# Kernel tuning notes

Measured on AMD Instinct MI355X. Metric: run time of the kernel, lower is better.

## Reference

```python
import jax, jax.numpy as jnp
import numpy as np

H = 16      # query heads
KV = 8      # kv heads
D = 128     # head_dim
HID = 2048  # hidden_size
T = 2048    # tokens
EPS = 1e-6
THETA = 1000000.0


def setup_inputs() -> dict:
    key = jax.random.key(0)
    ks = jax.random.split(key, 4)
    return {
        "hidden_states": jax.random.normal(ks[0], (T, HID), jnp.float32),
        "positions": jnp.arange(T, dtype=jnp.int32),
        "qkv_w": jax.random.normal(ks[1], (H * D + 2 * KV * D, HID), jnp.float32) * 0.02,
        "o_w": jax.random.normal(ks[2], (HID, H * D), jnp.float32) * 0.02,
        "q_norm_w": jnp.ones((D,), jnp.float32),
        "k_norm_w": jnp.ones((D,), jnp.float32),
    }


def _rmsnorm(x, w):
    # x: [T, heads, D]; normalize over last dim
    var = jnp.mean(x * x, axis=-1, keepdims=True)
    return x * jax.lax.rsqrt(var + EPS) * w


def _rope(x, positions):
    # neox-style rotate-half; x: [T, heads, D]
    half = D // 2
    inv_freq = 1.0 / (THETA ** (jnp.arange(0, half, dtype=jnp.float32) / half * 1.0))
    inv_freq = 1.0 / (THETA ** (jnp.arange(0, D, 2, dtype=jnp.float32) / D))
    ang = positions.astype(jnp.float32)[:, None] * inv_freq  # [T, D/2]
    cos = jnp.cos(ang)[:, None, :]
    sin = jnp.sin(ang)[:, None, :]
    x1, x2 = x[..., :half], x[..., half:]
    return jnp.concatenate([x1 * cos - x2 * sin, x2 * cos + x1 * sin], axis=-1)


def reference(hidden_states, positions, qkv_w, o_w, q_norm_w, k_norm_w):
    scale = D ** -0.5
    qkv = hidden_states @ qkv_w.T  # [T, H*D + 2*KV*D]
    q = qkv[:, : H * D].reshape(T, H, D)
    k = qkv[:, H * D : H * D + KV * D].reshape(T, KV, D)
    v = qkv[:, H * D + KV * D :].reshape(T, KV, D)

    q = _rope(_rmsnorm(q, q_norm_w), positions)
    k = _rope(_rmsnorm(k, k_norm_w), positions)

    # GQA: repeat kv heads to match query heads
    rep = H // KV
    k = jnp.repeat(k, rep, axis=1)  # [T, H, D]
    v = jnp.repeat(v, rep, axis=1)

    scores = jnp.einsum("thd,shd->hts", q, k) * scale  # [H, T, T]
    causal = positions[:, None] >= positions[None, :]  # [T, T]
    scores = jnp.where(causal[None, :, :], scores, jnp.float32(-1e30))
    p = jax.nn.softmax(scores, axis=-1)
    o = jnp.einsum("hts,shd->thd", p, v).reshape(T, H * D)
    return o @ o_w.T  # [T, HID]
```

## Files before the change

### kernel.cpp

```cpp
#include <hip/hip_runtime.h>
#include <math.h>

#define T_TOK 2048
#define HID 2048
#define NH 16
#define NKV 8
#define HD 128
#define QKV_N 4096
#define EPS 1e-6f

typedef unsigned short u16;
typedef unsigned int   u32;
typedef __attribute__((ext_vector_type(8))) u16   u16x8;
typedef __attribute__((ext_vector_type(8))) short short8;
typedef __attribute__((ext_vector_type(4))) float floatx4;
typedef __attribute__((ext_vector_type(4))) u32   u32x4;

__device__ __forceinline__ u16 f2bf(float x) {
    u32 u = __float_as_uint(x);
    u = (u + 0x7fffu + ((u >> 16) & 1u)) >> 16;
    return (u16)u;
}
__device__ __forceinline__ float bf2f(u16 h) {
    return __uint_as_float(((u32)h) << 16);
}

__global__ __launch_bounds__(256) void cvt_f32_bf16(
    const float* __restrict__ in, u16* __restrict__ out)
{
    const size_t i = ((size_t)blockIdx.x * 256 + threadIdx.x) * 8;
    float4 a = *(const float4*)(in + i);
    float4 b = *(const float4*)(in + i + 4);
    u16x8 o;
    o[0] = f2bf(a.x); o[1] = f2bf(a.y); o[2] = f2bf(a.z); o[3] = f2bf(a.w);
    o[4] = f2bf(b.x); o[5] = f2bf(b.y); o[6] = f2bf(b.z); o[7] = f2bf(b.w);
    *(u16x8*)(out + i) = o;
}

template<bool OUT_BF16>
__global__ __launch_bounds__(256) void gemm_bt_bf16(
    const u16* __restrict__ A, const u16* __restrict__ B,
    void* __restrict__ Cv, int K, int lda, int ldb, int ldc)
{
    __shared__ short As[128 * 32];
    __shared__ short Bs[128 * 32];

    const int tid = threadIdx.x;
    const int w   = tid >> 6;
    const int l   = tid & 63;
    const int m0  = blockIdx.y * 128;
    const int n0  = blockIdx.x * 128;
    const int wm  = (w >> 1) * 64;
    const int wn  = (w & 1) * 64;
    const int lm  = l & 15;
    const int ko8 = (l >> 4) * 8;

    const u16* gA0 = A + (size_t)(m0      + (tid >> 2)) * lda + (tid & 3) * 8;
    const u16* gA1 = A + (size_t)(m0 + 64 + (tid >> 2)) * lda + (tid & 3) * 8;
    const u16* gB0 = B + (size_t)(n0      + (tid >> 2)) * ldb + (tid & 3) * 8;
    const u16* gB1 = B + (size_t)(n0 + 64 + (tid >> 2)) * ldb + (tid & 3) * 8;
    short* lA0 = As + w * 512;
    short* lA1 = As + 2048 + w * 512;
    short* lB0 = Bs + w * 512;
    short* lB1 = Bs + 2048 + w * 512;

    floatx4 acc[4][4];
    #pragma unroll
    for (int i = 0; i < 4; ++i)
        #pragma unroll
        for (int j = 0; j < 4; ++j) acc[i][j] = (floatx4){0.f, 0.f, 0.f, 0.f};

    for (int k0 = 0; k0 < K; k0 += 32) {
        __syncthreads();
        __builtin_amdgcn_global_load_lds(
            (const __attribute__((address_space(1))) u32*)(gA0 + k0),
            (__attribute__((address_space(3))) u32*)lA0, 16, 0, 0);
        __builtin_amdgcn_global_load_lds(
            (const __attribute__((address_space(1))) u32*)(gA1 + k0),
            (__attribute__((address_space(3))) u32*)lA1, 16, 0, 0);
        __builtin_amdgcn_global_load_lds(
            (const __attribute__((address_space(1))) u32*)(gB0 + k0),
            (__attribute__((address_space(3))) u32*)lB0, 16, 0, 0);
        __builtin_amdgcn_global_load_lds(
            (const __attribute__((address_space(1))) u32*)(gB1 + k0),
            (__attribute__((address_space(3))) u32*)lB1, 16, 0, 0);
        __syncthreads();

        short8 af[4], bfr[4];
        #pragma unroll
        for (int i = 0; i < 4; ++i)
            af[i] = *(const short8*)(As + (wm + i * 16 + lm) * 32 + ko8);
        #pragma unroll
        for (int j = 0; j < 4; ++j)
            bfr[j] = *(const short8*)(Bs + (wn + j * 16 + lm) * 32 + ko8);
        #pragma unroll
        for (int i = 0; i < 4; ++i)
            #pragma unroll
            for (int j = 0; j < 4; ++j)
                acc[i][j] = __builtin_amdgcn_mfma_f32_16x16x32_bf16(
                    af[i], bfr[j], acc[i][j], 0, 0, 0);
    }

    const int r0 = (l >> 4) * 4;
    #pragma unroll
    for (int i = 0; i < 4; ++i)
        #pragma unroll
        for (int j = 0; j < 4; ++j)
            #pragma unroll
            for (int r = 0; r < 4; ++r) {
                const int row = m0 + wm + i * 16 + r0 + r;
                const int col = n0 + wn + j * 16 + lm;
                if (OUT_BF16)
                    ((u16*)Cv)[(size_t)row * ldc + col] = f2bf(acc[i][j][r]);
                else
                    ((float*)Cv)[(size_t)row * ldc + col] = acc[i][j][r];
            }
}

__global__ __launch_bounds__(256) void prep(
    u16* __restrict__ qkv, const int* __restrict__ positions,
    const float* __restrict__ qw, const float* __restrict__ kw,
    u16* __restrict__ Kp, u16* __restrict__ Vtp)
{
    const int tile = blockIdx.x, kvh = blockIdx.y;
    const int tid = threadIdx.x;
    const int w = tid >> 6, l = tid & 63;
    const int t0 = tile * 64;

    const float qw0 = qw[2*l], qw1 = qw[2*l+1];
    const float kw0 = kw[2*l], kw1 = kw[2*l+1];
    const int   i0  = (2*l) & 63;
    const float if0 = exp2f(-(float)i0     * 0.311430758895690f);
    const float if1 = exp2f(-(float)(i0+1) * 0.311430758895690f);

    for (int rr = w; rr < 64; rr += 4) {
        const int t = t0 + rr;
        const int pos = positions[t];
        const float a0 = (float)pos * if0;
        const float a1 = (float)pos * if1;
        const float s0 = sinf(a0), c0 = cosf(a0);
        const float s1 = sinf(a1), c1 = cosf(a1);

        #pragma unroll
        for (int pass = 0; pass < 3; ++pass) {
            const int off = (pass < 2) ? (2*kvh + pass)*HD : NH*HD + kvh*HD;
            const float w0 = (pass < 2) ? qw0 : kw0;
            const float w1 = (pass < 2) ? qw1 : kw1;
            u16* p = qkv + (size_t)t*QKV_N + off;

            const u32 pk = *(const u32*)(p + 2*l);
            const float x0 = bf2f((u16)pk), x1 = bf2f((u16)(pk >> 16));
            float ss = x0*x0 + x1*x1;
            #pragma unroll
            for (int x = 1; x < 64; x <<= 1) ss += __shfl_xor(ss, x);
            const float rs = rsqrtf(ss * (1.0f/128.0f) + EPS);
            const float xn0 = x0 * rs * w0, xn1 = x1 * rs * w1;
            const float px0 = __shfl_xor(xn0, 32);
            const float px1 = __shfl_xor(xn1, 32);

            float o0, o1;
            if (l < 32) { o0 = xn0*c0 - px0*s0; o1 = xn1*c1 - px1*s1; }
            else        { o0 = xn0*c0 + px0*s0; o1 = xn1*c1 + px1*s1; }
            const u32 outpk = (u32)f2bf(o0) | ((u32)f2bf(o1) << 16);

            if (pass < 2) {
                *(u32*)(p + 2*l) = outpk;
            } else {
                const int ch = l >> 2;
                u16* dst = Kp + ((size_t)(kvh*32 + tile)*64 + rr)*128
                              + (ch ^ (rr & 15))*8 + (l & 3)*2;
                *(u32*)dst = outpk;
            }
        }
    }

    __shared__ u16 tl[64][136];
    {
        const int t  = tid >> 2;
        const int c0 = (tid & 3) * 32;
        const u16* src = qkv + (size_t)(t0 + t)*QKV_N + NH*HD + NKV*HD + kvh*HD + c0;
        #pragma unroll
        for (int p2 = 0; p2 < 4; ++p2)
            *(u16x8*)(&tl[t][c0 + p2*8]) = *(const u16x8*)(src + p2*8);
    }
    __syncthreads();
    {
        u16* dstb = Vtp + (size_t)(kvh*32 + tile) * 128 * 64;
        #pragma unroll
        for (int i = 0; i < 4; ++i) {
            const int id = tid*4 + i;
            const int d = id >> 3;
            const int o = id & 7;
            const int sb = (o ^ (d & 7)) * 8;
            u16x8 v;
            #pragma unroll
            for (int j = 0; j < 8; ++j) v[j] = tl[sb + j][d];
            *(u16x8*)(dstb + d*64 + o*8) = v;
        }
    }
}

__global__ __launch_bounds__(512) void attn_mfma(
    const u16* __restrict__ qkv, const u16* __restrict__ Kp,
    const u16* __restrict__ Vtp,
    u16* __restrict__ Opart, float2* __restrict__ ml)
{
    const int id   = blockIdx.x;
    const int half = id >> 8;
    const int kvh  = id & 7;
    const int bid  = (id & 255) >> 3;
    const int qt   = half ? bid : 31 - bid;
    const int t0   = qt * 64;
    const int tid  = threadIdx.x;
    const int w    = tid >> 6;
    const int l    = tid & 63;
    const int q4   = l >> 4;
    const int c    = l & 15;
    const int h    = kvh*2 + (w >> 2);
    const int wq   = w & 3;

    __shared__ short Ks[2][64 * 128];
    __shared__ short Vts[2][128 * 64];

    short8 bq[4];
    {
        const u16* qrow = qkv + (size_t)(t0 + wq*16 + c) * QKV_N + h*HD;
        #pragma unroll
        for (int kk = 0; kk < 4; ++kk)
            bq[kk] = *(const short8*)(qrow + kk*32 + q4*8);
    }

    float m_run = -3.0e38f, l_run = 0.f;
    floatx4 accO[8];
    #pragma unroll
    for (int db = 0; db < 8; ++db) accO[db] = (floatx4){0.f, 0.f, 0.f, 0.f};

    const float Cs = 0.12751744f;

    const int nt  = qt + 1;
    const int nh0 = (nt + 1) >> 1;
    const int tlo = half ? nh0 : 0;
    const int thi = half ? nt  : nh0;

    auto issue = [&](int tile, int buf) {
        const size_t tb = (size_t)(kvh*32 + tile) * 8192;
        const u16* g = (w < 4 ? Kp + tb + w*2048 : Vtp + tb + (w-4)*2048) + l*8;
        short* p = (w < 4) ? (Ks[buf] + w*2048) : (Vts[buf] + (w-4)*2048);
        #pragma unroll
        for (int i = 0; i < 4; ++i)
            __builtin_amdgcn_global_load_lds(
                (const __attribute__((address_space(1))) u32*)(g + i*512),
                (__attribute__((address_space(3))) u32*)(p + i*512), 16, 0, 0);
    };

    if (tlo < thi) issue(tlo, 0);
    int cur = 0;

    for (int tile = tlo; tile < thi; ++tile) {
        __syncthreads();
        if (tile + 1 < thi) issue(tile + 1, cur ^ 1);

        const short* Kc = Ks[cur];
        const short* Vc = Vts[cur];

        floatx4 accS[4];
        #pragma unroll
        for (int sb = 0; sb < 4; ++sb) accS[sb] = (floatx4){0.f, 0.f, 0.f, 0.f};
        #pragma unroll
        for (int kk = 0; kk < 4; ++kk) {
            #pragma unroll
            for (int sb = 0; sb < 4; ++sb) {
                short8 ak = *(const short8*)(Kc + (sb*16 + c)*128 + ((kk*4 + q4) ^ c)*8);
                accS[sb] = __builtin_amdgcn_mfma_f32_16x16x32_bf16(ak, bq[kk], accS[sb], 0, 0, 0);
            }
        }

        if (tile == qt) {
            #pragma unroll
            for (int sb = 0; sb < 4; ++sb)
                #pragma unroll
                for (int r = 0; r < 4; ++r) {
                    const int s_loc = sb*16 + q4*4 + r;
                    const int t_loc = wq*16 + c;
                    if (s_loc > t_loc) accS[sb][r] = -1.0e30f;
                }
        }

        float mt = -3.0e38f;
        #pragma unroll
        for (int sb = 0; sb < 4; ++sb)
            #pragma unroll
            for (int r = 0; r < 4; ++r) mt = fmaxf(mt, accS[sb][r]);
        mt = fmaxf(mt, __shfl_xor(mt, 16));
        mt = fmaxf(mt, __shfl_xor(mt, 32));

        const float m_new = fmaxf(m_run, mt);
        const float alpha = exp2f((m_run - m_new) * Cs);
        m_run = m_new;

        float P[4][4];
        float lsum = 0.f;
        #pragma unroll
        for (int sb = 0; sb < 4; ++sb)
            #pragma unroll
            for (int r = 0; r < 4; ++r) {
                const float e = exp2f((accS[sb][r] - m_new) * Cs);
                P[sb][r] = e;
                lsum += e;
            }
        lsum += __shfl_xor(lsum, 16);
        lsum += __shfl_xor(lsum, 32);
        l_run = l_run * alpha + lsum;

        #pragma unroll
        for (int r = 0; r < 4; ++r) {
            const float ar = __shfl(alpha, (l & 48) | (q4*4 + r));
            #pragma unroll
            for (int db = 0; db < 8; ++db) accO[db][r] *= ar;
        }

        u32 Pp[4][2];
        #pragma unroll
        for (int sb = 0; sb < 4; ++sb)
            #pragma unroll
            for (int p = 0; p < 2; ++p)
                Pp[sb][p] = (u32)f2bf(P[sb][2*p]) | ((u32)f2bf(P[sb][2*p+1]) << 16);

        const int src0 = ((2*q4    ) & 3) * 16 + c;
        const int src1 = ((2*q4 + 1) & 3) * 16 + c;
        const bool hiq = q4 >= 2;
        #pragma unroll
        for (int k2 = 0; k2 < 2; ++k2) {
            u32 x0 = __shfl(Pp[2*k2][0],   src0), y0 = __shfl(Pp[2*k2+1][0], src0);
            u32 x1 = __shfl(Pp[2*k2][1],   src0), y1 = __shfl(Pp[2*k2+1][1], src0);
            u32 x2 = __shfl(Pp[2*k2][0],   src1), y2 = __shfl(Pp[2*k2+1][0], src1);
            u32 x3 = __shfl(Pp[2*k2][1],   src1), y3 = __shfl(Pp[2*k2+1][1], src1);
            u32x4 av;
            av.x = hiq ? y0 : x0;  av.y = hiq ? y1 : x1;
            av.z = hiq ? y2 : x2;  av.w = hiq ? y3 : x3;
            const short8 aP = __builtin_bit_cast(short8, av);
            #pragma unroll
            for (int db = 0; db < 8; ++db) {
                short8 bv = *(const short8*)(Vc + (db*16 + c)*64 + (((k2*4 + q4) ^ (c & 7)))*8);
                accO[db] = __builtin_amdgcn_mfma_f32_16x16x32_bf16(aP, bv, accO[db], 0, 0, 0);
            }
        }
        cur ^= 1;
    }

    const size_t pbase = (size_t)(half * NH + h) * T_TOK;
    #pragma unroll
    for (int r = 0; r < 4; ++r) {
        const int qloc = q4*4 + r;
        const float mr = __shfl(m_run, (l & 48) | qloc);
        const float lr = __shfl(l_run, (l & 48) | qloc);
        const int row_g = t0 + wq*16 + qloc;
        u16* op = Opart + (pbase + row_g) * HD;
        #pragma unroll
        for (int db = 0; db < 8; ++db)
            op[db*16 + c] = f2bf(accO[db][r]);
        if (c == 0) ml[pbase + row_g] = make_float2(mr, lr);
    }
}

__global__ __launch_bounds__(256) void attn_combine(
    const u16* __restrict__ Opart, const float2* __restrict__ ml,
    u16* __restrict__ qkv)
{
    const int idx = blockIdx.x * 256 + threadIdx.x;
    const int c16 = idx & 15;
    const int t   = (idx >> 4) & (T_TOK - 1);
    const int h   = idx >> 15;
    const size_t iA = (size_t)h * T_TOK + t;
    const size_t iB = (size_t)(NH + h) * T_TOK + t;
    const float2 a = ml[iA];
    const float2 b = ml[iB];
    const float Cs = 0.12751744f;
    const float mM = fmaxf(a.x, b.x);
    const float wA = exp2f((a.x - mM) * Cs);
    const float wB = exp2f((b.x - mM) * Cs);
    const float inv = 1.0f / (wA * a.y + wB * b.y);
    const u16x8 A = *(const u16x8*)(Opart + iA * HD + c16*8);
    const u16x8 B = *(const u16x8*)(Opart + iB * HD + c16*8);
    u16x8 o;
    #pragma unroll
    for (int j = 0; j < 8; ++j)
        o[j] = f2bf((wA * bf2f(A[j]) + wB * bf2f(B[j])) * inv);
    *(u16x8*)(qkv + (size_t)t * QKV_N + h * HD + c16*8) = o;
}

extern "C" void kernel_launch(void* const* d_in, const int* in_sizes, int n_in,
                              void* d_out, int out_size, void* d_ws, size_t ws_size,
                              hipStream_t stream)
{
    const float* hidden    = (const float*)d_in[0];
    const int*   positions = (const int*)  d_in[1];
    const float* qkv_w     = (const float*)d_in[2];
    const float* o_w       = (const float*)d_in[3];
    const float* q_norm_w  = (const float*)d_in[4];
    const float* k_norm_w  = (const float*)d_in[5];
    float* out = (float*)d_out;

    u16* qkvbf = (u16*)d_ws;
    u16* wbf   = qkvbf + (size_t)T_TOK * QKV_N;
    u16* abf   = wbf   + (size_t)QKV_N * HID;
    u16* kpb   = abf   + (size_t)T_TOK * HID;
    u16* vpb   = kpb   + (size_t)NKV * T_TOK * HD;

    cvt_f32_bf16<<<(T_TOK*HID)/2048, 256, 0, stream>>>(hidden, abf);
    cvt_f32_bf16<<<(QKV_N*HID)/2048, 256, 0, stream>>>(qkv_w, wbf);

    gemm_bt_bf16<true><<<dim3(QKV_N/128, T_TOK/128), 256, 0, stream>>>(
        abf, wbf, qkvbf, HID, HID, HID, QKV_N);

    prep<<<dim3(T_TOK/64, NKV), 256, 0, stream>>>(
        qkvbf, positions, q_norm_w, k_norm_w, kpb, vpb);

    attn_mfma<<<512, 512, 0, stream>>>(qkvbf, kpb, vpb, wbf, (float2*)abf);

    attn_combine<<<(NH*T_TOK*16)/256, 256, 0, stream>>>(
        wbf, (const float2*)abf, qkvbf);

    cvt_f32_bf16<<<(HID*HID)/2048, 256, 0, stream>>>(o_w, abf);
    gemm_bt_bf16<false><<<dim3(HID/128, T_TOK/128), 256, 0, stream>>>(
        qkvbf, abf, out, HID, QKV_N, HID, HID);
}
```

Before: 285.9 us.

## Replace GEMM with 256x128 triple-buffered, swizzled, 8-wave pipelined kernel

```diff
diff --git a/kernel.cpp b/kernel.cpp
--- a/kernel.cpp
+++ b/kernel.cpp
@@ -37,83 +37,137 @@
     *(u16x8*)(out + i) = o;
 }
 
+#define GBM 256
+#define GBN 128
+#define GBK 64
+#define BUFSH 24576
+
+#define WAITV6 asm volatile("s_waitcnt vmcnt(6)" ::: "memory")
+#define WAITV0 asm volatile("s_waitcnt vmcnt(0)" ::: "memory")
+#define LGKM0  asm volatile("s_waitcnt lgkmcnt(0)" ::: "memory")
+#define BARR   asm volatile("s_barrier" ::: "memory")
+#define SB     __builtin_amdgcn_sched_barrier(0)
+
+#define STAGEU(i, tt, dstb) \
+    __builtin_amdgcn_global_load_lds( \
+        (const __attribute__((address_space(1))) u32*)(gsrc[i] + (size_t)(tt)*GBK), \
+        (__attribute__((address_space(3))) u32*)((dstb) + loff[i]), 16, 0, 0)
+
+#define RD_A(dst, srcb, f) do { \
+    dst[0] = *(const short8*)((srcb) + arow + (f)*1024 + achunk0); \
+    dst[1] = *(const short8*)((srcb) + arow + (f)*1024 + achunk1); } while (0)
+
+#define RD_B(dst, srcb) do { \
+    _Pragma("unroll") \
+    for (int j_ = 0; j_ < 4; ++j_) { \
+        dst[j_][0] = *(const short8*)((srcb) + 16384 + brow + j_*1024 + achunk0); \
+        dst[j_][1] = *(const short8*)((srcb) + 16384 + brow + j_*1024 + achunk1); } } while (0)
+
+#define MM(f, aa, bb) do { \
+    __builtin_amdgcn_s_setprio(1); \
+    _Pragma("unroll") \
+    for (int j_ = 0; j_ < 4; ++j_) { \
+        acc[f][j_] = __builtin_amdgcn_mfma_f32_16x16x32_bf16(aa[0], bb[j_][0], acc[f][j_], 0, 0, 0); \
+        acc[f][j_] = __builtin_amdgcn_mfma_f32_16x16x32_bf16(aa[1], bb[j_][1], acc[f][j_], 0, 0, 0); } \
+    __builtin_amdgcn_s_setprio(0); } while (0)
+
+#define TILE(t, CURB, NXTB, THDB, BBC, BBN) do { \
+    const bool st_ = (t) + 2 < nt; \
+    if (st_) { STAGEU(0, (t)+2, THDB); STAGEU(1, (t)+2, THDB); } \
+    RD_A(aP1, CURB, 1); SB; \
+    MM(0, aP0, BBC); SB; \
+    if (st_) { STAGEU(2, (t)+2, THDB); STAGEU(3, (t)+2, THDB); } \
+    RD_A(aP0, CURB, 2); SB; \
+    MM(1, aP1, BBC); SB; \
+    if (st_) { STAGEU(4, (t)+2, THDB); STAGEU(5, (t)+2, THDB); } \
+    RD_A(aP1, CURB, 3); SB; \
+    MM(2, aP0, BBC); \
+    if ((t) + 1 < nt) { \
+        if (st_) { WAITV6; } else { WAITV0; } \
+        LGKM0; BARR; SB; \
+        RD_B(BBN, NXTB); RD_A(aP0, NXTB, 0); \
+    } \
+    SB; \
+    MM(3, aP1, BBC); SB; \
+} while (0)
+
 template<bool OUT_BF16>
-__global__ __launch_bounds__(256) void gemm_bt_bf16(
+__global__ __launch_bounds__(512, 2) void gemm_bt_8p(
     const u16* __restrict__ A, const u16* __restrict__ B,
     void* __restrict__ Cv, int K, int lda, int ldb, int ldc)
 {
-    __shared__ short As[128 * 32];
-    __shared__ short Bs[128 * 32];
-
+    extern __shared__ short lds[];
     const int tid = threadIdx.x;
-    const int w   = tid >> 6;
-    const int l   = tid & 63;
-    const int m0  = blockIdx.y * 128;
-    const int n0  = blockIdx.x * 128;
-    const int wm  = (w >> 1) * 64;
-    const int wn  = (w & 1) * 64;
-    const int lm  = l & 15;
-    const int ko8 = (l >> 4) * 8;
-
-    const u16* gA0 = A + (size_t)(m0      + (tid >> 2)) * lda + (tid & 3) * 8;
-    const u16* gA1 = A + (size_t)(m0 + 64 + (tid >> 2)) * lda + (tid & 3) * 8;
-    const u16* gB0 = B + (size_t)(n0      + (tid >> 2)) * ldb + (tid & 3) * 8;
-    const u16* gB1 = B + (size_t)(n0 + 64 + (tid >> 2)) * ldb + (tid & 3) * 8;
-    short* lA0 = As + w * 512;
-    short* lA1 = As + 2048 + w * 512;
-    short* lB0 = Bs + w * 512;
-    short* lB1 = Bs + 2048 + w * 512;
+    const int w  = tid >> 6;
+    const int l  = tid & 63;
+    const int m0 = blockIdx.y * GBM;
+    const int n0 = blockIdx.x * GBN;
+    const int mr = (w >> 1) * 64;
+    const int nc = (w & 1) * 64;
+    const int cc = l & 15;
+    const int q4 = l >> 4;
+
+    const int lr = l >> 3;
+    const int gchunk = ((l & 7) ^ (lr & 7)) * 8;
+    const u16* gsrc[6]; int loff[6];
+    #pragma unroll
+    for (int i = 0; i < 6; ++i) {
+        const int u = w * 6 + i;
+        if (u < 32) {
+            gsrc[i] = A + (size_t)(m0 + u*8 + lr) * lda + gchunk;
+            loff[i] = u * 512;
+        } else {
+            const int v = u - 32;
+            gsrc[i] = B + (size_t)(n0 + v*8 + lr) * ldb + gchunk;
+            loff[i] = 16384 + v * 512;
+        }
+    }
+
+    const int achunk0 = ((q4)     ^ (cc & 7)) * 8;
+    const int achunk1 = ((4 + q4) ^ (cc & 7)) * 8;
+    const int arow = (mr + cc) * 64;
+    const int brow = (nc + cc) * 64;
 
     floatx4 acc[4][4];
     #pragma unroll
-    for (int i = 0; i < 4; ++i)
-        #pragma unroll
-        for (int j = 0; j < 4; ++j) acc[i][j] = (floatx4){0.f, 0.f, 0.f, 0.f};
-
-    for (int k0 = 0; k0 < K; k0 += 32) {
-        __syncthreads();
-        __builtin_amdgcn_global_load_lds(
-            (const __attribute__((address_space(1))) u32*)(gA0 + k0),
-            (__attribute__((address_space(3))) u32*)lA0, 16, 0, 0);
-        __builtin_amdgcn_global_load_lds(
-            (const __attribute__((address_space(1))) u32*)(gA1 + k0),
-            (__attribute__((address_space(3))) u32*)lA1, 16, 0, 0);
-        __builtin_amdgcn_global_load_lds(
-            (const __attribute__((address_space(1))) u32*)(gB0 + k0),
-            (__attribute__((address_space(3))) u32*)lB0, 16, 0, 0);
-        __builtin_amdgcn_global_load_lds(
-            (const __attribute__((address_space(1))) u32*)(gB1 + k0),
-            (__attribute__((address_space(3))) u32*)lB1, 16, 0, 0);
-        __syncthreads();
-
-        short8 af[4], bfr[4];
-        #pragma unroll
-        for (int i = 0; i < 4; ++i)
-            af[i] = *(const short8*)(As + (wm + i * 16 + lm) * 32 + ko8);
+    for (int f = 0; f < 4; ++f)
+        #pragma unroll
+        for (int j = 0; j < 4; ++j) acc[f][j] = (floatx4){0.f, 0.f, 0.f, 0.f};
+
+    short8 aP0[2], aP1[2], bbE[4][2], bbO[4][2];
+    short* b0 = lds;
+    short* b1 = lds + BUFSH;
+    short* b2 = lds + 2 * BUFSH;
+    const int nt = K >> 6;
+
+    #pragma unroll
+    for (int i = 0; i < 6; ++i) STAGEU(i, 0, b0);
+    #pragma unroll
+    for (int i = 0; i < 6; ++i) STAGEU(i, 1, b1);
+    WAITV6; BARR; SB;
+    RD_B(bbE, b0); RD_A(aP0, b0, 0);
+
+    short *CURB = b0, *NXTB = b1, *THDB = b2;
+    for (int t = 0; t < nt; t += 2) {
+        TILE(t, CURB, NXTB, THDB, bbE, bbO);
+        { short* tmp = CURB; CURB = NXTB; NXTB = THDB; THDB = tmp; }
+        TILE(t + 1, CURB, NXTB, THDB, bbO, bbE);
+        { short* tmp = CURB; CURB = NXTB; NXTB = THDB; THDB = tmp; }
+    }
+
+    const int r0 = q4 * 4;
+    #pragma unroll
+    for (int f = 0; f < 4; ++f)
         #pragma unroll
         for (int j = 0; j < 4; ++j)
-            bfr[j] = *(const short8*)(Bs + (wn + j * 16 + lm) * 32 + ko8);
-        #pragma unroll
-        for (int i = 0; i < 4; ++i)
-            #pragma unroll
-            for (int j = 0; j < 4; ++j)
-                acc[i][j] = __builtin_amdgcn_mfma_f32_16x16x32_bf16(
-                    af[i], bfr[j], acc[i][j], 0, 0, 0);
-    }
-
-    const int r0 = (l >> 4) * 4;
-    #pragma unroll
-    for (int i = 0; i < 4; ++i)
-        #pragma unroll
-        for (int j = 0; j < 4; ++j)
             #pragma unroll
             for (int r = 0; r < 4; ++r) {
-                const int row = m0 + wm + i * 16 + r0 + r;
-                const int col = n0 + wn + j * 16 + lm;
+                const int row = m0 + mr + f*16 + r0 + r;
+                const int col = n0 + nc + j*16 + cc;
                 if (OUT_BF16)
-                    ((u16*)Cv)[(size_t)row * ldc + col] = f2bf(acc[i][j][r]);
+                    ((u16*)Cv)[(size_t)row * ldc + col] = f2bf(acc[f][j][r]);
                 else
-                    ((float*)Cv)[(size_t)row * ldc + col] = acc[i][j][r];
+                    ((float*)Cv)[(size_t)row * ldc + col] = acc[f][j][r];
             }
 }
 
@@ -407,10 +461,21 @@
     u16* kpb   = abf   + (size_t)T_TOK * HID;
     u16* vpb   = kpb   + (size_t)NKV * T_TOK * HD;
 
+    static bool s_attr = false;
+    if (!s_attr) {
+        (void)hipFuncSetAttribute(
+            reinterpret_cast<const void*>(&gemm_bt_8p<true>),
+            hipFuncAttributeMaxDynamicSharedMemorySize, 147456);
+        (void)hipFuncSetAttribute(
+            reinterpret_cast<const void*>(&gemm_bt_8p<false>),
+            hipFuncAttributeMaxDynamicSharedMemorySize, 147456);
+        s_attr = true;
+    }
+
     cvt_f32_bf16<<<(T_TOK*HID)/2048, 256, 0, stream>>>(hidden, abf);
     cvt_f32_bf16<<<(QKV_N*HID)/2048, 256, 0, stream>>>(qkv_w, wbf);
 
-    gemm_bt_bf16<true><<<dim3(QKV_N/128, T_TOK/128), 256, 0, stream>>>(
+    gemm_bt_8p<true><<<dim3(QKV_N/GBN, T_TOK/GBM), 512, 147456, stream>>>(
         abf, wbf, qkvbf, HID, HID, HID, QKV_N);
 
     prep<<<dim3(T_TOK/64, NKV), 256, 0, stream>>>(
@@ -422,6 +487,6 @@
         wbf, (const float2*)abf, qkvbf);
 
     cvt_f32_bf16<<<(HID*HID)/2048, 256, 0, stream>>>(o_w, abf);
-    gemm_bt_bf16<false><<<dim3(HID/128, T_TOK/128), 256, 0, stream>>>(
+    gemm_bt_8p<false><<<dim3(HID/GBN, T_TOK/GBM), 512, 147456, stream>>>(
         qkvbf, abf, out, HID, QKV_N, HID, HID);
 }
```

Result: faster. 248.9 us (-12.9%).
